# Optimization experiments

Measured on AMD Instinct MI355X. Metric: run time of the kernel, lower is better.

Reference implementation:

```python
import jax, jax.numpy as jnp
import numpy as np

H = 2048          # hidden_size
E = 8             # num_experts
TOP_K = 2         # num_experts_per_tok
I_MOE = 1408      # moe_intermediate_size
I_SH = 5632       # shared_expert_intermediate_size
BS, NT = 2, 512   # batch, tokens per seq


def setup_inputs() -> dict:
    key = jax.random.key(0)
    ks = jax.random.split(key, 7)
    s = lambda d: (1.0 / np.sqrt(d)).astype(np.float32)
    return {
        "hidden_states": jax.random.normal(ks[0], (BS, NT, H), jnp.float32),
        "gate_w": jax.random.normal(ks[1], (E, H), jnp.float32) * s(H),
        "w1": jax.random.normal(ks[2], (E, 2 * I_MOE, H), jnp.float32) * s(H),   # per-expert gate_up
        "w2": jax.random.normal(ks[3], (E, H, I_MOE), jnp.float32) * s(I_MOE),   # per-expert down
        "shared_gate_up_w": jax.random.normal(ks[4], (2 * I_SH, H), jnp.float32) * s(H),
        "shared_down_w": jax.random.normal(ks[5], (H, I_SH), jnp.float32) * s(I_SH),
        "shared_gate_w": jax.random.normal(ks[6], (1, H), jnp.float32) * s(H),
    }


def reference(hidden_states, gate_w, w1, w2, shared_gate_up_w, shared_down_w, shared_gate_w):
    bs, nt, h = hidden_states.shape
    x = hidden_states.reshape(-1, h)                      # [T, H]
    T = x.shape[0]

    # shared expert (WeLMMoeMLP: gate_up -> SiluAndMul -> down), gated by sigmoid
    gu = x @ shared_gate_up_w.T                           # [T, 2*I_SH]
    g, u = jnp.split(gu, 2, axis=-1)
    shared = (jax.nn.silu(g) * u) @ shared_down_w.T       # [T, H]
    shared = jax.nn.sigmoid(x @ shared_gate_w.T) * shared

    # router: softmax -> top_k -> renormalize (norm_topk_prob=True)
    logits = x @ gate_w.T                                 # [T, E]
    probs = jax.nn.softmax(logits.astype(jnp.float32), axis=-1)
    top_w, top_i = jax.lax.top_k(probs, TOP_K)            # [T, K]
    top_w = top_w / jnp.sum(top_w, axis=-1, keepdims=True)
    combine = jnp.zeros((T, E), top_w.dtype).at[jnp.arange(T)[:, None], top_i].set(top_w)

    # experts: per-expert gate_up -> SiluAndMul -> down, weighted combine
    gu_e = jnp.einsum('th,eih->tei', x, w1)               # [T, E, 2*I_MOE]
    ge, ue = jnp.split(gu_e, 2, axis=-1)
    he = jax.nn.silu(ge) * ue                             # [T, E, I_MOE]
    ye = jnp.einsum('tei,ehi->teh', he, w2)               # [T, E, H]
    out = jnp.einsum('teh,te->th', ye, combine.astype(x.dtype)) + shared
    return out.reshape(bs, nt, h)
```

## Files before the change

### kernel.cpp

```cpp
#include <hip/hip_runtime.h>
#include <hip/hip_bf16.h>
#include <math.h>

#define HID   2048
#define NEXP  8
#define IMOE  1408
#define ISH   5632
#define NTOK  1024
#define NASSIGN 2048

typedef __bf16 bf16;
typedef __bf16 bf16x4 __attribute__((ext_vector_type(4)));
typedef __bf16 bf16x8 __attribute__((ext_vector_type(8)));
typedef float  f32x4  __attribute__((ext_vector_type(4)));

__device__ inline void async16(const bf16* g, bf16* l) {
  __builtin_amdgcn_global_load_lds(
      (const __attribute__((address_space(1))) void*)g,
      (__attribute__((address_space(3))) void*)l, 16, 0, 0);
}

#define CC0 256L
#define CC1 5888L
#define CC2 8704L
#define CC3 11520L
#define CC4 12928L
#define CVT_BLOCKS 2048

__global__ __launch_bounds__(256) void convert_kernel(
    const float* __restrict__ x, const float* __restrict__ w1,
    const float* __restrict__ w2, const float* __restrict__ sgu,
    const float* __restrict__ sdw,
    bf16* __restrict__ xb, bf16* __restrict__ w1b, bf16* __restrict__ w2b,
    bf16* __restrict__ sgub, bf16* __restrict__ sdwb)
{
  const int tid = threadIdx.x;
  for (long c = blockIdx.x; c < CC4; c += CVT_BLOCKS) {
    const float* s; bf16* d; long off;
    if      (c < CC0) { s = x;   d = xb;   off = c; }
    else if (c < CC1) { s = w1;  d = w1b;  off = c - CC0; }
    else if (c < CC2) { s = w2;  d = w2b;  off = c - CC1; }
    else if (c < CC3) { s = sgu; d = sgub; off = c - CC2; }
    else              { s = sdw; d = sdwb; off = c - CC3; }
    long base = off * 8192 + (long)tid * 4;
    f32x4 v[8];
#pragma unroll
    for (int sub = 0; sub < 8; sub++)
      v[sub] = __builtin_nontemporal_load((const f32x4*)(s + base + sub * 1024));
#pragma unroll
    for (int sub = 0; sub < 8; sub++) {
      bf16x4 r;
      r[0] = (bf16)v[sub][0]; r[1] = (bf16)v[sub][1];
      r[2] = (bf16)v[sub][2]; r[3] = (bf16)v[sub][3];
      *(bf16x4*)(d + base + sub * 1024) = r;
    }
  }
}

__global__ __launch_bounds__(256) void router_kernel(
    const float* __restrict__ x, const float* __restrict__ gate_w,
    const float* __restrict__ sgate_w, float* __restrict__ sg,
    int2* __restrict__ tk_idx, float2* __restrict__ tk_w)
{
  const int t = blockIdx.x;
  const float* xr = x + (long)t * HID;
  float p[9];
#pragma unroll
  for (int i = 0; i < 9; i++) p[i] = 0.f;
  for (int c = threadIdx.x; c < HID; c += 256) {
    float xv = xr[c];
#pragma unroll
    for (int e = 0; e < 8; e++) p[e] += xv * gate_w[e * HID + c];
    p[8] += xv * sgate_w[c];
  }
#pragma unroll
  for (int i = 0; i < 9; i++)
    for (int off = 32; off > 0; off >>= 1)
      p[i] += __shfl_xor(p[i], off, 64);
  __shared__ float red[4][9];
  const int wave = threadIdx.x >> 6, lane = threadIdx.x & 63;
  if (lane == 0)
    for (int i = 0; i < 9; i++) red[wave][i] = p[i];
  __syncthreads();
  if (threadIdx.x == 0) {
    float l[9];
    for (int i = 0; i < 9; i++)
      l[i] = red[0][i] + red[1][i] + red[2][i] + red[3][i];
    int i0 = 0;
    for (int e = 1; e < 8; e++) if (l[e] > l[i0]) i0 = e;
    int i1 = -1;
    for (int e = 0; e < 8; e++) {
      if (e == i0) continue;
      if (i1 < 0 || l[e] > l[i1]) i1 = e;
    }
    float w0 = 1.f / (1.f + __expf(l[i1] - l[i0]));
    tk_idx[t] = make_int2(i0, i1);
    tk_w[t]   = make_float2(w0, 1.f - w0);
    sg[t]     = 1.f / (1.f + __expf(-l[8]));
  }
}

__global__ __launch_bounds__(256) void scatter_kernel(
    const int2* __restrict__ tk_idx, const float2* __restrict__ tk_w,
    int* __restrict__ offs, int* __restrict__ s_tok, float* __restrict__ s_wgt)
{
  __shared__ int cnt[8], pos[8];
  if (threadIdx.x < 8) cnt[threadIdx.x] = 0;
  __syncthreads();
  for (int a = threadIdx.x; a < NASSIGN; a += 256) {
    int2 ii = tk_idx[a >> 1];
    int e = (a & 1) ? ii.y : ii.x;
    atomicAdd(&cnt[e], 1);
  }
  __syncthreads();
  if (threadIdx.x == 0) {
    int s = 0;
    for (int e = 0; e < 8; e++) { offs[e] = s; pos[e] = s; s += cnt[e]; }
    offs[8] = s;
  }
  __syncthreads();
  for (int a = threadIdx.x; a < NASSIGN; a += 256) {
    int t = a >> 1;
    int2 ii = tk_idx[t];
    float2 ww = tk_w[t];
    int   e = (a & 1) ? ii.y : ii.x;
    float w = (a & 1) ? ww.y : ww.x;
    int pp = atomicAdd(&pos[e], 1);
    s_tok[pp] = t;
    s_wgt[pp] = w;
  }
}

template<int BM, bool GROUPED>
__global__ __launch_bounds__(256) void gemm_gu(
    const bf16* __restrict__ X,
    const bf16* __restrict__ Wg_base, long expert_stride, long up_off,
    bf16* __restrict__ Hout, int hstride,
    const int* __restrict__ offs, const int* __restrict__ s_tok,
    const bf16* __restrict__ zpad)
{
  static_assert(BM == 64 || BM == 128, "BM");
  constexpr int K = HID, NS = K / 32;
  constexpr int AIP = BM / 64;
  constexpr int AF  = BM / 32;
  const int n0 = blockIdx.x * 64;
  const int e  = GROUPED ? blockIdx.z : 0;
  int m_base, m_end;
  if (GROUPED) {
    m_base = offs[e] + blockIdx.y * BM;
    m_end  = offs[e + 1];
    if (m_base >= m_end) return;
  } else { m_base = blockIdx.y * BM; m_end = NTOK; }
  const bf16* Wg = Wg_base + (long)e * expert_stride;

  __shared__ __attribute__((aligned(16))) bf16 As[BM * 32];
  __shared__ __attribute__((aligned(16))) bf16 Bs[128 * 32];

  const int tid = threadIdx.x, wave = tid >> 6, lane = tid & 63;

  const bf16* pa[AIP]; bf16* la[AIP];
#pragma unroll
  for (int q = 0; q < AIP; q++) {
    int ia  = wave * AIP + q;
    int rl  = ia * 16 + (lane >> 2);
    int gch = (lane & 3) ^ (rl & 3);
    const bf16* src;
    if (GROUPED) {
      int gr  = m_base + rl;
      int tok = (gr < m_end) ? s_tok[gr] : -1;
      src = (tok >= 0) ? X + (long)tok * K : zpad;
    } else src = X + (long)(m_base + rl) * K;
    pa[q] = src + gch * 8;
    la[q] = As + ia * 512;
  }
  const bf16* pb[2]; bf16* lb[2];
#pragma unroll
  for (int q = 0; q < 2; q++) {
    int ib  = wave * 2 + q;
    int rl  = ib * 16 + (lane >> 2);
    int gch = (lane & 3) ^ (rl & 3);
    const bf16* src = (rl < 64) ? Wg + (long)(n0 + rl) * K
                                : Wg + up_off + (long)(n0 + rl - 64) * K;
    pb[q] = src + gch * 8;
    lb[q] = Bs + ib * 512;
  }

  const int wm = wave >> 1, wn = wave & 1;
  f32x4 accg[AF][2], accu[AF][2];
#pragma unroll
  for (int i = 0; i < AF; i++)
#pragma unroll
    for (int j = 0; j < 2; j++) {
      accg[i][j] = f32x4{0.f, 0.f, 0.f, 0.f};
      accu[i][j] = f32x4{0.f, 0.f, 0.f, 0.f};
    }

  const int fr = lane & 15, cch = lane >> 4;

  for (int s = 0; s < NS; s++) {
    __syncthreads();
#pragma unroll
    for (int q = 0; q < AIP; q++) { async16(pa[q], la[q]); pa[q] += 32; }
#pragma unroll
    for (int q = 0; q < 2;   q++) { async16(pb[q], lb[q]); pb[q] += 32; }
    asm volatile("s_waitcnt vmcnt(0)" ::: "memory");
    __syncthreads();

    bf16x8 a[AF], bg[2], bu[2];
#pragma unroll
    for (int i = 0; i < AF; i++) {
      int ar = wm * (AF * 16) + i * 16 + fr;
      a[i] = *(const bf16x8*)&As[ar * 32 + ((cch ^ (ar & 3)) * 8)];
    }
#pragma unroll
    for (int j = 0; j < 2; j++) {
      int br = wn * 32 + j * 16 + fr;
      int ur = 64 + br;
      bg[j] = *(const bf16x8*)&Bs[br * 32 + ((cch ^ (br & 3)) * 8)];
      bu[j] = *(const bf16x8*)&Bs[ur * 32 + ((cch ^ (ur & 3)) * 8)];
    }
#pragma unroll
    for (int i = 0; i < AF; i++)
#pragma unroll
      for (int j = 0; j < 2; j++) {
        accg[i][j] = __builtin_amdgcn_mfma_f32_16x16x32_bf16(a[i], bg[j], accg[i][j], 0, 0, 0);
        accu[i][j] = __builtin_amdgcn_mfma_f32_16x16x32_bf16(a[i], bu[j], accu[i][j], 0, 0, 0);
      }
  }
#pragma unroll
  for (int i = 0; i < AF; i++)
#pragma unroll
    for (int j = 0; j < 2; j++)
#pragma unroll
      for (int r = 0; r < 4; r++) {
        int row  = wm * (AF * 16) + i * 16 + (lane >> 4) * 4 + r;
        int grow = m_base + row;
        if (GROUPED && grow >= m_end) continue;
        int col = wn * 32 + j * 16 + (lane & 15);
        float g = accg[i][j][r], u = accu[i][j][r];
        float h = g / (1.f + __expf(-g)) * u;
        Hout[(long)grow * hstride + n0 + col] = (bf16)h;
      }
}

template<int BM, bool GROUPED, int KSPLIT>
__global__ __launch_bounds__(256) void gemm_down(
    const bf16* __restrict__ Hin, int K,
    const bf16* __restrict__ W_base, long expert_stride,
    float* __restrict__ Out, const float* __restrict__ scale,
    const int* __restrict__ offs, const int* __restrict__ s_tok)
{
  static_assert(BM == 64 || BM == 128, "BM");
  constexpr int AIP = BM / 64, AF = BM / 32;
  const int n0 = blockIdx.x * 128;
  int e = 0, ks, m_base, m_end;
  if (GROUPED) {
    e  = blockIdx.z / KSPLIT;
    ks = blockIdx.z % KSPLIT;
    m_base = offs[e] + blockIdx.y * BM;
    m_end  = offs[e + 1];
    if (m_base >= m_end) return;
  } else {
    ks = blockIdx.z;
    m_base = blockIdx.y * BM;
    m_end  = NTOK;
  }
  const int k_lo = ks * (K / KSPLIT);
  const int NS   = (K / KSPLIT) / 32;
  const bf16* W = W_base + (long)e * expert_stride;

  __shared__ __attribute__((aligned(16))) bf16 As[BM * 32];
  __shared__ __attribute__((aligned(16))) bf16 Bs[128 * 32];

  const int tid = threadIdx.x, wave = tid >> 6, lane = tid & 63;

  const bf16* pa[AIP]; bf16* la[AIP];
#pragma unroll
  for (int q = 0; q < AIP; q++) {
    int ia  = wave * AIP + q;
    int rl  = ia * 16 + (lane >> 2);
    int gch = (lane & 3) ^ (rl & 3);
    pa[q] = Hin + (long)(m_base + rl) * K + k_lo + gch * 8;
    la[q] = As + ia * 512;
  }
  const bf16* pb[2]; bf16* lb[2];
#pragma unroll
  for (int q = 0; q < 2; q++) {
    int ib  = wave * 2 + q;
    int rl  = ib * 16 + (lane >> 2);
    int gch = (lane & 3) ^ (rl & 3);
    pb[q] = W + (long)(n0 + rl) * K + k_lo + gch * 8;
    lb[q] = Bs + ib * 512;
  }

  const int wm = wave >> 1, wn = wave & 1;
  f32x4 acc[AF][4];
#pragma unroll
  for (int i = 0; i < AF; i++)
#pragma unroll
    for (int j = 0; j < 4; j++) acc[i][j] = f32x4{0.f, 0.f, 0.f, 0.f};

  const int fr = lane & 15, cch = lane >> 4;

  for (int s = 0; s < NS; s++) {
    __syncthreads();
#pragma unroll
    for (int q = 0; q < AIP; q++) { async16(pa[q], la[q]); pa[q] += 32; }
#pragma unroll
    for (int q = 0; q < 2;   q++) { async16(pb[q], lb[q]); pb[q] += 32; }
    asm volatile("s_waitcnt vmcnt(0)" ::: "memory");
    __syncthreads();

    bf16x8 a[AF], b[4];
#pragma unroll
    for (int i = 0; i < AF; i++) {
      int ar = wm * (AF * 16) + i * 16 + fr;
      a[i] = *(const bf16x8*)&As[ar * 32 + ((cch ^ (ar & 3)) * 8)];
    }
#pragma unroll
    for (int j = 0; j < 4; j++) {
      int br = wn * 64 + j * 16 + fr;
      b[j] = *(const bf16x8*)&Bs[br * 32 + ((cch ^ (br & 3)) * 8)];
    }
#pragma unroll
    for (int i = 0; i < AF; i++)
#pragma unroll
      for (int j = 0; j < 4; j++)
        acc[i][j] = __builtin_amdgcn_mfma_f32_16x16x32_bf16(a[i], b[j], acc[i][j], 0, 0, 0);
  }
#pragma unroll
  for (int i = 0; i < AF; i++)
#pragma unroll
    for (int j = 0; j < 4; j++)
#pragma unroll
      for (int r = 0; r < 4; r++) {
        int row  = wm * (AF * 16) + i * 16 + (lane >> 4) * 4 + r;
        int grow = m_base + row;
        if (GROUPED && grow >= m_end) continue;
        int col = wn * 64 + j * 16 + (lane & 15);
        float sc = scale[grow];
        int target = GROUPED ? s_tok[grow] : grow;
        atomicAdd(&Out[(long)target * HID + n0 + col], sc * acc[i][j][r]);
      }
}

extern "C" void kernel_launch(void* const* d_in, const int* in_sizes, int n_in,
                              void* d_out, int out_size, void* d_ws, size_t ws_size,
                              hipStream_t stream)
{
  const float* x    = (const float*)d_in[0];
  const float* gw   = (const float*)d_in[1];
  const float* w1   = (const float*)d_in[2];
  const float* w2   = (const float*)d_in[3];
  const float* sguw = (const float*)d_in[4];
  const float* sdw  = (const float*)d_in[5];
  const float* sgw  = (const float*)d_in[6];
  float* out = (float*)d_out;

  char* ws = (char*)d_ws;
  size_t off = 0;
  auto alloc = [&](size_t bytes) {
    void* p = ws + off;
    off = (off + bytes + 255) & ~(size_t)255;
    return p;
  };
  float*  sg    = (float*)alloc(NTOK * 4);
  int2*   tki   = (int2*)alloc(NTOK * 8);
  float2* tkw   = (float2*)alloc(NTOK * 8);
  int*    offs  = (int*)alloc(64);
  int*    s_tok = (int*)alloc(NASSIGN * 4);
  float*  s_wgt = (float*)alloc(NASSIGN * 4);
  bf16*   zpadb = (bf16*)alloc((HID + 64) * 2);
  bf16*   xb    = (bf16*)alloc((size_t)NTOK * HID * 2);
  bf16*   w1b   = (bf16*)alloc((size_t)NEXP * 2 * IMOE * HID * 2);
  bf16*   w2b   = (bf16*)alloc((size_t)NEXP * HID * IMOE * 2);
  bf16*   sgub  = (bf16*)alloc((size_t)2 * ISH * HID * 2);
  bf16*   sdwb  = (bf16*)alloc((size_t)HID * ISH * 2);
  bf16*   h_sh  = (bf16*)alloc((size_t)NTOK * ISH * 2);
  bf16*   h_e   = (bf16*)alloc((size_t)(NASSIGN + 128) * IMOE * 2);

  hipMemsetAsync(zpadb, 0, (HID + 64) * 2, stream);
  hipMemsetAsync(d_out, 0, (size_t)out_size * 4, stream);
  router_kernel<<<NTOK, 256, 0, stream>>>(x, gw, sgw, sg, tki, tkw);
  scatter_kernel<<<1, 256, 0, stream>>>(tki, tkw, offs, s_tok, s_wgt);
  convert_kernel<<<CVT_BLOCKS, 256, 0, stream>>>(x, w1, w2, sguw, sdw,
                                                 xb, w1b, w2b, sgub, sdwb);

  gemm_gu<128, false><<<dim3(ISH / 64, NTOK / 128, 1), 256, 0, stream>>>(
      xb, sgub, 0, (long)ISH * HID, h_sh, ISH, nullptr, nullptr, zpadb);
  gemm_gu<128, true><<<dim3(IMOE / 64, 16, NEXP), 256, 0, stream>>>(
      xb, w1b, (long)2 * IMOE * HID, (long)IMOE * HID, h_e, IMOE, offs, s_tok, zpadb);
  gemm_down<128, false, 8><<<dim3(HID / 128, NTOK / 128, 8), 256, 0, stream>>>(
      h_sh, ISH, sdwb, 0, out, sg, nullptr, nullptr);
  gemm_down<128, true, 2><<<dim3(HID / 128, 16, NEXP * 2), 256, 0, stream>>>(
      h_e, IMOE, w2b, (long)HID * IMOE, out, s_wgt, offs, s_tok);
}
```

Baseline: 673.7 us.

## Merge shared and expert GEMMs into single launches with swizzled block order

The shared-expert and routed-expert gate_up GEMMs now run in one launch, and the two down GEMMs run in another, by decoding a flat block index into either the shared or the grouped expert tile. Shared tiles use a swizzled block order so that neighbouring blocks reuse the same weight and activation tiles in cache. The shared down projection now splits K four ways instead of eight. The aim is to remove launch gaps and tail underutilisation between the separate GEMMs, at the cost of runtime branching on the grouped flag and fewer but longer shared-down blocks.

```diff
diff --git a/kernel.cpp b/kernel.cpp
--- a/kernel.cpp
+++ b/kernel.cpp
@@ -18,6 +18,14 @@
   __builtin_amdgcn_global_load_lds(
       (const __attribute__((address_space(1))) void*)g,
       (__attribute__((address_space(3))) void*)l, 16, 0, 0);
+}
+
+__device__ inline void swz_decode(int s, int cxn, int& bx, int& by) {
+  int p  = (s >> 3) & 7;
+  int c  = (s & 7) + ((s >> 6) << 3);
+  int cx = c % cxn, cy = c / cxn;
+  bx = cx * 4 + (p & 3);
+  by = cy * 2 + (p >> 2);
 }
 
 #define CC0 256L
@@ -131,41 +139,25 @@
   }
 }
 
-template<int BM, bool GROUPED>
-__global__ __launch_bounds__(256) void gemm_gu(
+__device__ __forceinline__ void gu_core(
+    bf16* __restrict__ As, bf16* __restrict__ Bs,
     const bf16* __restrict__ X,
-    const bf16* __restrict__ Wg_base, long expert_stride, long up_off,
+    const bf16* __restrict__ Wg, long up_off,
     bf16* __restrict__ Hout, int hstride,
-    const int* __restrict__ offs, const int* __restrict__ s_tok,
-    const bf16* __restrict__ zpad)
-{
-  static_assert(BM == 64 || BM == 128, "BM");
+    const int* __restrict__ s_tok, const bf16* __restrict__ zpad,
+    bool grouped, int m_base, int m_end, int n0)
+{
   constexpr int K = HID, NS = K / 32;
-  constexpr int AIP = BM / 64;
-  constexpr int AF  = BM / 32;
-  const int n0 = blockIdx.x * 64;
-  const int e  = GROUPED ? blockIdx.z : 0;
-  int m_base, m_end;
-  if (GROUPED) {
-    m_base = offs[e] + blockIdx.y * BM;
-    m_end  = offs[e + 1];
-    if (m_base >= m_end) return;
-  } else { m_base = blockIdx.y * BM; m_end = NTOK; }
-  const bf16* Wg = Wg_base + (long)e * expert_stride;
-
-  __shared__ __attribute__((aligned(16))) bf16 As[BM * 32];
-  __shared__ __attribute__((aligned(16))) bf16 Bs[128 * 32];
-
   const int tid = threadIdx.x, wave = tid >> 6, lane = tid & 63;
 
-  const bf16* pa[AIP]; bf16* la[AIP];
-#pragma unroll
-  for (int q = 0; q < AIP; q++) {
-    int ia  = wave * AIP + q;
+  const bf16* pa[2]; bf16* la[2];
+#pragma unroll
+  for (int q = 0; q < 2; q++) {
+    int ia  = wave * 2 + q;
     int rl  = ia * 16 + (lane >> 2);
     int gch = (lane & 3) ^ (rl & 3);
     const bf16* src;
-    if (GROUPED) {
+    if (grouped) {
       int gr  = m_base + rl;
       int tok = (gr < m_end) ? s_tok[gr] : -1;
       src = (tok >= 0) ? X + (long)tok * K : zpad;
@@ -186,9 +178,9 @@
   }
 
   const int wm = wave >> 1, wn = wave & 1;
-  f32x4 accg[AF][2], accu[AF][2];
-#pragma unroll
-  for (int i = 0; i < AF; i++)
+  f32x4 accg[4][2], accu[4][2];
+#pragma unroll
+  for (int i = 0; i < 4; i++)
 #pragma unroll
     for (int j = 0; j < 2; j++) {
       accg[i][j] = f32x4{0.f, 0.f, 0.f, 0.f};
@@ -200,16 +192,16 @@
   for (int s = 0; s < NS; s++) {
     __syncthreads();
 #pragma unroll
-    for (int q = 0; q < AIP; q++) { async16(pa[q], la[q]); pa[q] += 32; }
-#pragma unroll
-    for (int q = 0; q < 2;   q++) { async16(pb[q], lb[q]); pb[q] += 32; }
+    for (int q = 0; q < 2; q++) { async16(pa[q], la[q]); pa[q] += 32; }
+#pragma unroll
+    for (int q = 0; q < 2; q++) { async16(pb[q], lb[q]); pb[q] += 32; }
     asm volatile("s_waitcnt vmcnt(0)" ::: "memory");
     __syncthreads();
 
-    bf16x8 a[AF], bg[2], bu[2];
-#pragma unroll
-    for (int i = 0; i < AF; i++) {
-      int ar = wm * (AF * 16) + i * 16 + fr;
+    bf16x8 a[4], bg[2], bu[2];
+#pragma unroll
+    for (int i = 0; i < 4; i++) {
+      int ar = wm * 64 + i * 16 + fr;
       a[i] = *(const bf16x8*)&As[ar * 32 + ((cch ^ (ar & 3)) * 8)];
     }
 #pragma unroll
@@ -220,7 +212,7 @@
       bu[j] = *(const bf16x8*)&Bs[ur * 32 + ((cch ^ (ur & 3)) * 8)];
     }
 #pragma unroll
-    for (int i = 0; i < AF; i++)
+    for (int i = 0; i < 4; i++)
 #pragma unroll
       for (int j = 0; j < 2; j++) {
         accg[i][j] = __builtin_amdgcn_mfma_f32_16x16x32_bf16(a[i], bg[j], accg[i][j], 0, 0, 0);
@@ -228,14 +220,14 @@
       }
   }
 #pragma unroll
-  for (int i = 0; i < AF; i++)
+  for (int i = 0; i < 4; i++)
 #pragma unroll
     for (int j = 0; j < 2; j++)
 #pragma unroll
       for (int r = 0; r < 4; r++) {
-        int row  = wm * (AF * 16) + i * 16 + (lane >> 4) * 4 + r;
+        int row  = wm * 64 + i * 16 + (lane >> 4) * 4 + r;
         int grow = m_base + row;
-        if (GROUPED && grow >= m_end) continue;
+        if (grow >= m_end) continue;
         int col = wn * 32 + j * 16 + (lane & 15);
         float g = accg[i][j][r], u = accu[i][j][r];
         float h = g / (1.f + __expf(-g)) * u;
@@ -243,41 +235,55 @@
       }
 }
 
-template<int BM, bool GROUPED, int KSPLIT>
-__global__ __launch_bounds__(256) void gemm_down(
-    const bf16* __restrict__ Hin, int K,
-    const bf16* __restrict__ W_base, long expert_stride,
+#define GU_SH_BLOCKS 704
+#define GU_E_X 22
+#define GU_BLOCKS (GU_SH_BLOCKS + GU_E_X * 16 * NEXP)
+
+__global__ __launch_bounds__(256) void gemm_gu_fused(
+    const bf16* __restrict__ X,
+    const bf16* __restrict__ sgu, const bf16* __restrict__ w1,
+    bf16* __restrict__ Hsh, bf16* __restrict__ He,
+    const int* __restrict__ offs, const int* __restrict__ s_tok,
+    const bf16* __restrict__ zpad)
+{
+  __shared__ __attribute__((aligned(16))) bf16 As[128 * 32];
+  __shared__ __attribute__((aligned(16))) bf16 Bs[128 * 32];
+  const int bid = blockIdx.x;
+  const bf16* Wg; long up_off; bf16* Hout; int hstride;
+  int n0, m_base, m_end; bool grouped;
+  if (bid < GU_SH_BLOCKS) {
+    int bx, by; swz_decode(bid, 22, bx, by);
+    n0 = bx * 64; m_base = by * 128; m_end = NTOK;
+    Wg = sgu; up_off = (long)ISH * HID;
+    Hout = Hsh; hstride = ISH; grouped = false;
+  } else {
+    int r = bid - GU_SH_BLOCKS;
+    int bx = r % GU_E_X; r /= GU_E_X;
+    int by = r % 16; int e = r / 16;
+    m_base = offs[e] + by * 128; m_end = offs[e + 1];
+    if (m_base >= m_end) return;
+    n0 = bx * 64;
+    Wg = w1 + (long)e * (2L * IMOE * HID); up_off = (long)IMOE * HID;
+    Hout = He; hstride = IMOE; grouped = true;
+  }
+  gu_core(As, Bs, X, Wg, up_off, Hout, hstride, s_tok, zpad,
+          grouped, m_base, m_end, n0);
+}
+
+__device__ __forceinline__ void down_core(
+    bf16* __restrict__ As, bf16* __restrict__ Bs,
+    const bf16* __restrict__ Hin, int K, int k_lo, int NS,
+    const bf16* __restrict__ W,
     float* __restrict__ Out, const float* __restrict__ scale,
-    const int* __restrict__ offs, const int* __restrict__ s_tok)
-{
-  static_assert(BM == 64 || BM == 128, "BM");
-  constexpr int AIP = BM / 64, AF = BM / 32;
-  const int n0 = blockIdx.x * 128;
-  int e = 0, ks, m_base, m_end;
-  if (GROUPED) {
-    e  = blockIdx.z / KSPLIT;
-    ks = blockIdx.z % KSPLIT;
-    m_base = offs[e] + blockIdx.y * BM;
-    m_end  = offs[e + 1];
-    if (m_base >= m_end) return;
-  } else {
-    ks = blockIdx.z;
-    m_base = blockIdx.y * BM;
-    m_end  = NTOK;
-  }
-  const int k_lo = ks * (K / KSPLIT);
-  const int NS   = (K / KSPLIT) / 32;
-  const bf16* W = W_base + (long)e * expert_stride;
-
-  __shared__ __attribute__((aligned(16))) bf16 As[BM * 32];
-  __shared__ __attribute__((aligned(16))) bf16 Bs[128 * 32];
-
+    const int* __restrict__ s_tok, bool grouped,
+    int m_base, int m_end, int n0)
+{
   const int tid = threadIdx.x, wave = tid >> 6, lane = tid & 63;
 
-  const bf16* pa[AIP]; bf16* la[AIP];
-#pragma unroll
-  for (int q = 0; q < AIP; q++) {
-    int ia  = wave * AIP + q;
+  const bf16* pa[2]; bf16* la[2];
+#pragma unroll
+  for (int q = 0; q < 2; q++) {
+    int ia  = wave * 2 + q;
     int rl  = ia * 16 + (lane >> 2);
     int gch = (lane & 3) ^ (rl & 3);
     pa[q] = Hin + (long)(m_base + rl) * K + k_lo + gch * 8;
@@ -294,9 +300,9 @@
   }
 
   const int wm = wave >> 1, wn = wave & 1;
-  f32x4 acc[AF][4];
-#pragma unroll
-  for (int i = 0; i < AF; i++)
+  f32x4 acc[4][4];
+#pragma unroll
+  for (int i = 0; i < 4; i++)
 #pragma unroll
     for (int j = 0; j < 4; j++) acc[i][j] = f32x4{0.f, 0.f, 0.f, 0.f};
 
@@ -305,16 +311,16 @@
   for (int s = 0; s < NS; s++) {
     __syncthreads();
 #pragma unroll
-    for (int q = 0; q < AIP; q++) { async16(pa[q], la[q]); pa[q] += 32; }
-#pragma unroll
-    for (int q = 0; q < 2;   q++) { async16(pb[q], lb[q]); pb[q] += 32; }
+    for (int q = 0; q < 2; q++) { async16(pa[q], la[q]); pa[q] += 32; }
+#pragma unroll
+    for (int q = 0; q < 2; q++) { async16(pb[q], lb[q]); pb[q] += 32; }
     asm volatile("s_waitcnt vmcnt(0)" ::: "memory");
     __syncthreads();
 
-    bf16x8 a[AF], b[4];
-#pragma unroll
-    for (int i = 0; i < AF; i++) {
-      int ar = wm * (AF * 16) + i * 16 + fr;
+    bf16x8 a[4], b[4];
+#pragma unroll
+    for (int i = 0; i < 4; i++) {
+      int ar = wm * 64 + i * 16 + fr;
       a[i] = *(const bf16x8*)&As[ar * 32 + ((cch ^ (ar & 3)) * 8)];
     }
 #pragma unroll
@@ -323,25 +329,61 @@
       b[j] = *(const bf16x8*)&Bs[br * 32 + ((cch ^ (br & 3)) * 8)];
     }
 #pragma unroll
-    for (int i = 0; i < AF; i++)
+    for (int i = 0; i < 4; i++)
 #pragma unroll
       for (int j = 0; j < 4; j++)
         acc[i][j] = __builtin_amdgcn_mfma_f32_16x16x32_bf16(a[i], b[j], acc[i][j], 0, 0, 0);
   }
 #pragma unroll
-  for (int i = 0; i < AF; i++)
+  for (int i = 0; i < 4; i++)
 #pragma unroll
     for (int j = 0; j < 4; j++)
 #pragma unroll
       for (int r = 0; r < 4; r++) {
-        int row  = wm * (AF * 16) + i * 16 + (lane >> 4) * 4 + r;
+        int row  = wm * 64 + i * 16 + (lane >> 4) * 4 + r;
         int grow = m_base + row;
-        if (GROUPED && grow >= m_end) continue;
+        if (grow >= m_end) continue;
         int col = wn * 64 + j * 16 + (lane & 15);
         float sc = scale[grow];
-        int target = GROUPED ? s_tok[grow] : grow;
+        int target = grouped ? s_tok[grow] : grow;
         atomicAdd(&Out[(long)target * HID + n0 + col], sc * acc[i][j][r]);
       }
+}
+
+#define DN_SH_BLOCKS 512
+#define DN_BLOCKS (DN_SH_BLOCKS + 16 * 16 * NEXP * 2)
+
+__global__ __launch_bounds__(256) void gemm_down_fused(
+    const bf16* __restrict__ Hsh, const bf16* __restrict__ He,
+    const bf16* __restrict__ sdw, const bf16* __restrict__ w2,
+    float* __restrict__ Out, const float* __restrict__ sg,
+    const float* __restrict__ s_wgt,
+    const int* __restrict__ offs, const int* __restrict__ s_tok)
+{
+  __shared__ __attribute__((aligned(16))) bf16 As[128 * 32];
+  __shared__ __attribute__((aligned(16))) bf16 Bs[128 * 32];
+  const int bid = blockIdx.x;
+  const bf16* Hin; const bf16* W; const float* scale;
+  int K, k_lo, NS, m_base, m_end, n0; bool grouped;
+  if (bid < DN_SH_BLOCKS) {
+    int plane = bid >> 7;
+    int bx, by; swz_decode(bid & 127, 4, bx, by);
+    Hin = Hsh; K = ISH; k_lo = plane * (ISH / 4); NS = (ISH / 4) / 32;
+    W = sdw; scale = sg; grouped = false;
+    m_base = by * 128; m_end = NTOK; n0 = bx * 128;
+  } else {
+    int r = bid - DN_SH_BLOCKS;
+    int bx = r % 16; r /= 16;
+    int by = r % 16; r /= 16;
+    int e = r >> 1, ks = r & 1;
+    m_base = offs[e] + by * 128; m_end = offs[e + 1];
+    if (m_base >= m_end) return;
+    Hin = He; K = IMOE; k_lo = ks * (IMOE / 2); NS = (IMOE / 2) / 32;
+    W = w2 + (long)e * HID * IMOE; scale = s_wgt; grouped = true;
+    n0 = bx * 128;
+  }
+  down_core(As, Bs, Hin, K, k_lo, NS, W, Out, scale, s_tok, grouped,
+            m_base, m_end, n0);
 }
 
 extern "C" void kernel_launch(void* const* d_in, const int* in_sizes, int n_in,
@@ -386,12 +428,8 @@
   convert_kernel<<<CVT_BLOCKS, 256, 0, stream>>>(x, w1, w2, sguw, sdw,
                                                  xb, w1b, w2b, sgub, sdwb);
 
-  gemm_gu<128, false><<<dim3(ISH / 64, NTOK / 128, 1), 256, 0, stream>>>(
-      xb, sgub, 0, (long)ISH * HID, h_sh, ISH, nullptr, nullptr, zpadb);
-  gemm_gu<128, true><<<dim3(IMOE / 64, 16, NEXP), 256, 0, stream>>>(
-      xb, w1b, (long)2 * IMOE * HID, (long)IMOE * HID, h_e, IMOE, offs, s_tok, zpadb);
-  gemm_down<128, false, 8><<<dim3(HID / 128, NTOK / 128, 8), 256, 0, stream>>>(
-      h_sh, ISH, sdwb, 0, out, sg, nullptr, nullptr);
-  gemm_down<128, true, 2><<<dim3(HID / 128, 16, NEXP * 2), 256, 0, stream>>>(
-      h_e, IMOE, w2b, (long)HID * IMOE, out, s_wgt, offs, s_tok);
-}
+  gemm_gu_fused<<<GU_BLOCKS, 256, 0, stream>>>(
+      xb, sgub, w1b, h_sh, h_e, offs, s_tok, zpadb);
+  gemm_down_fused<<<DN_BLOCKS, 256, 0, stream>>>(
+      h_sh, h_e, sdwb, w2b, out, sg, s_wgt, offs, s_tok);
+}
```

After: 643.1 us. 4.5% less time.
